# Optimization experiments

Measured on AMD Instinct MI355X. Metric: run time of the kernel, lower is better.

The kernel has to match this reference:

```python
import jax, jax.numpy as jnp
import numpy as np
import math

B, S, HID, H = 4, 2048, 1024, 16
D = HID // H


def setup_inputs() -> dict:
    key = jax.random.key(0)
    ks = jax.random.split(key, 13)
    xavier = lambda k: jax.random.normal(k, (HID, HID), jnp.float32) * math.sqrt(2.0 / (HID + HID))
    return {
        "q": jax.random.normal(ks[0], (B, S, HID), jnp.float32),
        "k": jax.random.normal(ks[1], (B, S, HID), jnp.float32),
        "v": jax.random.normal(ks[2], (B, S, HID), jnp.float32),
        "padding_mask": jax.random.randint(ks[3], (B, S), 0, 2, jnp.int32),
        "Wq": xavier(ks[4]), "bq": jnp.zeros((HID,), jnp.float32),
        "Wk": xavier(ks[5]), "bk": jnp.zeros((HID,), jnp.float32),
        "Wv": xavier(ks[6]), "bv": jnp.zeros((HID,), jnp.float32),
        "Wo": xavier(ks[7]), "bo": jnp.zeros((HID,), jnp.float32),
        "is_causal": 1,
    }


def reference(q, k, v, padding_mask, Wq, bq, Wk, bk, Wv, bv, Wo, bo, is_causal):
    b, s, _ = q.shape
    # torch Linear: y = x @ W.T + b; reshape to [B, H, S, D]
    proj = lambda x, W, bias: (x @ W.T + bias).reshape(b, s, H, D).transpose(0, 2, 1, 3)
    qh, kh, vh = proj(q, Wq, bq), proj(k, Wk, bk), proj(v, Wv, bv)
    corr = jnp.einsum("bhqd,bhkd->bhqk", qh, kh) / math.sqrt(D)  # [B,H,S,S]
    # padding_mask.view(B,1,S,1): masks QUERY rows where mask == 0 (faithful to source)
    corr = jnp.where(padding_mask[:, None, :, None] == 0, jnp.float32(-1e9), corr)
    if is_causal:
        # triu -inf above diagonal; where(...) equals corr + (-inf) at masked slots
        tri = jnp.triu(jnp.ones((s, s), bool), k=1)
        corr = jnp.where(tri[None, None], -jnp.inf, corr)
    prob = jax.nn.softmax(corr, axis=-1)  # dropout p=0 (eval)
    hidden = jnp.einsum("bhqk,bhkd->bhqd", prob, vh)  # [B,H,S,D]
    hidden = hidden.transpose(0, 2, 1, 3).reshape(b, s, H * D)
    return hidden @ Wo.T + bo
```

## Files before the change

kernel.cpp:

```cpp
#include <hip/hip_runtime.h>
#include <hip/hip_bf16.h>
#include <stdint.h>

typedef __attribute__((ext_vector_type(8))) short bf16x8;
typedef __attribute__((ext_vector_type(4))) float f32x4;
typedef __attribute__((ext_vector_type(16))) float f32x16;
typedef __attribute__((ext_vector_type(8))) unsigned short ushort8;
typedef __attribute__((ext_vector_type(4))) unsigned short ushort4v;
typedef __attribute__((ext_vector_type(4))) unsigned int u32x4;
typedef __attribute__((ext_vector_type(2))) unsigned int u32x2;

#define DEVINL __device__ __forceinline__

static constexpr int BB  = 4;
static constexpr int SS  = 2048;
static constexpr int HID = 1024;
static constexpr int NH  = 16;
static constexpr int DH  = 64;

DEVINL unsigned short f2bf(float f) {
  unsigned u = __builtin_bit_cast(unsigned, f);
  u += 0x7fffu + ((u >> 16) & 1u);
  return (unsigned short)(u >> 16);
}

DEVINL unsigned cvt_pk_bf16(float lo, float hi) {
  unsigned r;
  asm("v_cvt_pk_bf16_f32 %0, %1, %2" : "=v"(r) : "v"(lo), "v"(hi));
  return r;
}

DEVINL void gload_lds16(const void* g, void* lds) {
  __builtin_amdgcn_global_load_lds(
      (__attribute__((address_space(1))) unsigned int*)(g),
      (__attribute__((address_space(3))) unsigned int*)(lds), 16, 0, 0);
}

__global__ void cvt4_weights(const float* __restrict__ a,
                             const float* __restrict__ b,
                             const float* __restrict__ c,
                             const float* __restrict__ d,
                             unsigned short* __restrict__ dst) {
  int which = blockIdx.x >> 10;
  const float* src = which == 0 ? a : which == 1 ? b : which == 2 ? c : d;
  int i = ((blockIdx.x & 1023) * 256 + threadIdx.x) * 4;
  float4 v = *(const float4*)(src + i);
  ushort4v h;
  h.x = f2bf(v.x); h.y = f2bf(v.y); h.z = f2bf(v.z); h.w = f2bf(v.w);
  *(ushort4v*)(dst + which * 1048576 + i) = h;
}

__launch_bounds__(256)
__global__ void gemm_qkv(const float* __restrict__ qp,
                         const float* __restrict__ kp,
                         const float* __restrict__ vp,
                         const unsigned short* __restrict__ W,
                         const float* __restrict__ bq,
                         const float* __restrict__ bk,
                         const float* __restrict__ bv,
                         unsigned short* __restrict__ dstQK,
                         unsigned short* __restrict__ Vt, float sclq) {
  __shared__ __align__(16) unsigned char As[16384];
  __shared__ __align__(16) unsigned char Bs[16384];
  const int cpx = gridDim.x >> 3;
  const int bid = (blockIdx.x & 7) * cpx + (blockIdx.x >> 3);
  const int which = bid / 512;
  const int tile = bid - which * 512;
  const int bm = tile >> 3, bn = tile & 7;
  const int m0 = bm << 7, n0 = bn << 7;
  const int K = 1024, N = 1024;
  const float* Af = which == 0 ? qp : which == 1 ? kp : vp;
  const unsigned short* Bw = W + which * 1048576;
  const float* bias = which == 0 ? bq : which == 1 ? bk : bv;
  const float osc = which == 0 ? sclq : 1.0f;

  const int t = threadIdx.x, lane = t & 63, wv = t >> 6;
  const int wr = wv >> 1, wc = wv & 1;
  const int l15 = lane & 15, l4 = lane >> 4;

  f32x4 acc[4][4] = {};

  for (int k0 = 0; k0 < K; k0 += 64) {
#pragma unroll
    for (int j = 0; j < 4; ++j) {
      int p = (wv * 4 + j) * 1024 + lane * 16;
      int row = p >> 7;
      int cb = (p & 127) ^ ((row & 7) << 4);
      gload_lds16(Bw + (size_t)(n0 + row) * K + k0 + (cb >> 1),
                  Bs + (wv * 4 + j) * 1024);
    }
#pragma unroll
    for (int j = 0; j < 8; ++j) {
      int qid = t + j * 256;
      int row = qid >> 4;
      int q16 = qid & 15;
      float4 v = *(const float4*)(Af + (size_t)(m0 + row) * K + k0 + q16 * 4);
      u32x2 w;
      w.x = cvt_pk_bf16(v.x, v.y);
      w.y = cvt_pk_bf16(v.z, v.w);
      int byte = (row * 128 + q16 * 8) ^ ((row & 7) << 4);
      *(u32x2*)(As + byte) = w;
    }
    asm volatile("s_waitcnt vmcnt(0)" ::: "memory");
    __syncthreads();

    bf16x8 af[2][4], bfr[2][4];
#pragma unroll
    for (int kh = 0; kh < 2; ++kh) {
#pragma unroll
      for (int m = 0; m < 4; ++m) {
        int r = wr * 64 + m * 16 + l15;
        int byte = (r * 128 + kh * 64 + l4 * 16) ^ ((r & 7) << 4);
        af[kh][m] = *(const bf16x8*)(As + byte);
      }
#pragma unroll
      for (int n = 0; n < 4; ++n) {
        int r = wc * 64 + n * 16 + l15;
        int byte = (r * 128 + kh * 64 + l4 * 16) ^ ((r & 7) << 4);
        bfr[kh][n] = *(const bf16x8*)(Bs + byte);
      }
    }
#pragma unroll
    for (int kh = 0; kh < 2; ++kh)
#pragma unroll
      for (int m = 0; m < 4; ++m)
#pragma unroll
        for (int n = 0; n < 4; ++n)
          acc[m][n] = __builtin_amdgcn_mfma_f32_16x16x32_bf16(
              af[kh][m], bfr[kh][n], acc[m][n], 0, 0, 0);
    __syncthreads();
  }

  if (which < 2) {
    unsigned short* Cp = dstQK + (size_t)which * 8388608;
#pragma unroll
    for (int n = 0; n < 4; ++n) {
      int col = n0 + wc * 64 + n * 16 + l15;
      float bc = bias[col];
#pragma unroll
      for (int m = 0; m < 4; ++m) {
        int rowb = m0 + wr * 64 + m * 16 + l4 * 4;
#pragma unroll
        for (int r = 0; r < 4; ++r) {
          float val = (acc[m][n][r] + bc) * osc;
          Cp[(size_t)(rowb + r) * N + col] = f2bf(val);
        }
      }
    }
  } else {
#pragma unroll
    for (int n = 0; n < 4; ++n) {
      int dcol = n0 + wc * 64 + n * 16 + l15;
      float bc = bias[dcol];
#pragma unroll
      for (int m = 0; m < 4; ++m) {
        int srow = m0 + wr * 64 + m * 16 + l4 * 4;
        int bb = srow >> 11, s = srow & 2047;
        ushort4v o;
#pragma unroll
        for (int r = 0; r < 4; ++r) o[r] = f2bf(acc[m][n][r] + bc);
        *(ushort4v*)(Vt + ((size_t)(bb * 1024 + dcol)) * 2048 + s) = o;
      }
    }
  }
}

__launch_bounds__(256)
__global__ void gemm_out(const unsigned short* __restrict__ Ab,
                         const unsigned short* __restrict__ Bw,
                         const float* __restrict__ bias,
                         float* __restrict__ Cp, int M, int N, int K) {
  __shared__ __align__(16) unsigned char As[16384];
  __shared__ __align__(16) unsigned char Bs[16384];
  const int cpx = gridDim.x >> 3;
  const int bid = (blockIdx.x & 7) * cpx + (blockIdx.x >> 3);
  const int nb = N >> 7;
  const int bm = bid / nb, bn = bid % nb;
  const int m0 = bm << 7, n0 = bn << 7;
  const int t = threadIdx.x, lane = t & 63, wv = t >> 6;
  const int wr = wv >> 1, wc = wv & 1;
  const int l15 = lane & 15, l4 = lane >> 4;

  f32x4 acc[4][4] = {};

  for (int k0 = 0; k0 < K; k0 += 64) {
#pragma unroll
    for (int j = 0; j < 4; ++j) {
      int p = (wv * 4 + j) * 1024 + lane * 16;
      int row = p >> 7;
      int cb = (p & 127) ^ ((row & 7) << 4);
      gload_lds16(Bw + (size_t)(n0 + row) * K + k0 + (cb >> 1),
                  Bs + (wv * 4 + j) * 1024);
      gload_lds16(Ab + (size_t)(m0 + row) * K + k0 + (cb >> 1),
                  As + (wv * 4 + j) * 1024);
    }
    asm volatile("s_waitcnt vmcnt(0)" ::: "memory");
    __syncthreads();

    bf16x8 af[2][4], bfr[2][4];
#pragma unroll
    for (int kh = 0; kh < 2; ++kh) {
#pragma unroll
      for (int m = 0; m < 4; ++m) {
        int r = wr * 64 + m * 16 + l15;
        int byte = (r * 128 + kh * 64 + l4 * 16) ^ ((r & 7) << 4);
        af[kh][m] = *(const bf16x8*)(As + byte);
      }
#pragma unroll
      for (int n = 0; n < 4; ++n) {
        int r = wc * 64 + n * 16 + l15;
        int byte = (r * 128 + kh * 64 + l4 * 16) ^ ((r & 7) << 4);
        bfr[kh][n] = *(const bf16x8*)(Bs + byte);
      }
    }
#pragma unroll
    for (int kh = 0; kh < 2; ++kh)
#pragma unroll
      for (int m = 0; m < 4; ++m)
#pragma unroll
        for (int n = 0; n < 4; ++n)
          acc[m][n] = __builtin_amdgcn_mfma_f32_16x16x32_bf16(
              af[kh][m], bfr[kh][n], acc[m][n], 0, 0, 0);
    __syncthreads();
  }

#pragma unroll
  for (int n = 0; n < 4; ++n) {
    int col = n0 + wc * 64 + n * 16 + l15;
    float bc = bias[col];
#pragma unroll
    for (int m = 0; m < 4; ++m) {
      int rowb = m0 + wr * 64 + m * 16 + l4 * 4;
#pragma unroll
      for (int r = 0; r < 4; ++r)
        Cp[(size_t)(rowb + r) * N + col] = acc[m][n][r] + bc;
    }
  }
}

__launch_bounds__(256)
__global__ void attn_kernel(const unsigned short* __restrict__ Qh,
                            const unsigned short* __restrict__ Kh,
                            const unsigned short* __restrict__ Vt,
                            const int* __restrict__ pad,
                            const int* __restrict__ pcausal,
                            unsigned short* __restrict__ Out) {
  __shared__ __align__(16) unsigned char Ks[2][16384];
  __shared__ __align__(16) unsigned char Vs[2][16384];
  const int bid = (blockIdx.x & 7) * 64 + (blockIdx.x >> 3);
  const int pr = bid & 7, h = (bid >> 3) & 15, b = bid >> 7;
  const int t = threadIdx.x, lane = t & 63, wv = t >> 6;
  const int l31 = lane & 31, hi = lane >> 5;
  const int causal = *pcausal;

  for (int half = 0; half < 2; ++half) {
    const int qt = half ? (15 - pr) : pr;
    const int q0 = qt << 7;
    const int qrow = q0 + wv * 32 + l31;
    const bool padded = (pad[b * SS + qrow] == 0);

    const unsigned short* Qb = Qh + ((size_t)(b * SS) + qrow) * HID + h * DH;
    bf16x8 qf[4];
#pragma unroll
    for (int dd = 0; dd < 4; ++dd) {
      qf[dd] = *(const bf16x8*)(Qb + dd * 16 + hi * 8);
      if (padded) qf[dd] = (bf16x8)0;
    }

    f32x16 oacc[2] = {};
    float m = -__builtin_inff(), l = 0.f;
    const int nkt = causal ? (qt + 1) : (SS >> 7);

    auto STAGE = [&](int kt, int s) {
#pragma unroll
      for (int j = 0; j < 4; ++j) {
        int p = (wv * 4 + j) * 1024 + lane * 16;
        int kr = p >> 7;
        int kcb = (p & 127) ^ ((kr & 7) << 4);
        gload_lds16(Kh + ((size_t)(b * SS) + (kt << 7) + kr) * HID + h * DH +
                        (kcb >> 1),
                    Ks[s] + (wv * 4 + j) * 1024);
        int vr = p >> 8;
        int vcb = (p & 255) ^ ((vr & 15) << 4);
        gload_lds16(Vt + ((size_t)((b * NH + h) * DH + vr)) * SS + (kt << 7) +
                        (vcb >> 1),
                    Vs[s] + (wv * 4 + j) * 1024);
      }
    };

    if (half) __syncthreads();
    STAGE(0, 0);
    for (int kt = 0; kt < nkt; ++kt) {
      asm volatile("s_waitcnt vmcnt(0)" ::: "memory");
      __syncthreads();
      if (kt + 1 < nkt) STAGE(kt + 1, (kt + 1) & 1);
      const unsigned char* Kb = Ks[kt & 1];
      const unsigned char* Vb = Vs[kt & 1];

#pragma unroll
      for (int sub = 0; sub < 2; ++sub) {
        const int k0 = (kt << 7) + (sub << 6);
        const bool active = (!causal) || (k0 <= q0 + wv * 32 + 31);
        if (!active) continue;
        f32x16 sacc[2] = {};
#pragma unroll
        for (int kb = 0; kb < 2; ++kb) {
#pragma unroll
          for (int dd = 0; dd < 4; ++dd) {
            int krow = sub * 64 + kb * 32 + l31;
            int byte = (krow * 128 + dd * 32 + hi * 16) ^ ((krow & 7) << 4);
            bf16x8 kf = *(const bf16x8*)(Kb + byte);
            sacc[kb] = __builtin_amdgcn_mfma_f32_32x32x16_bf16(kf, qf[dd],
                                                               sacc[kb], 0, 0, 0);
          }
        }
        if (causal && (k0 + 63 > q0 + wv * 32)) {
#pragma unroll
          for (int kb = 0; kb < 2; ++kb)
#pragma unroll
            for (int r = 0; r < 16; ++r) {
              int kidx = k0 + kb * 32 + (r & 3) + 8 * (r >> 2) + 4 * hi;
              if (kidx > qrow) sacc[kb][r] = -__builtin_inff();
            }
        }
        float ta = fmaxf(sacc[0][0], sacc[0][1]);
        float tb = fmaxf(sacc[0][2], sacc[0][3]);
#pragma unroll
        for (int r = 4; r < 16; r += 4) {
          ta = fmaxf(ta, fmaxf(sacc[0][r], sacc[0][r + 1]));
          tb = fmaxf(tb, fmaxf(sacc[0][r + 2], sacc[0][r + 3]));
        }
#pragma unroll
        for (int r = 0; r < 16; r += 4) {
          ta = fmaxf(ta, fmaxf(sacc[1][r], sacc[1][r + 1]));
          tb = fmaxf(tb, fmaxf(sacc[1][r + 2], sacc[1][r + 3]));
        }
        float tmax = fmaxf(ta, tb);
        tmax = fmaxf(tmax, __shfl_xor(tmax, 32));
        if (__any(tmax > m + 8.0f)) {
          float mnew = fmaxf(m, tmax);
          float corr = __builtin_amdgcn_exp2f(m - mnew);
          m = mnew;
          l *= corr;
#pragma unroll
          for (int db = 0; db < 2; ++db)
#pragma unroll
            for (int r = 0; r < 16; ++r) oacc[db][r] *= corr;
        }
        float ls = 0.f;
#pragma unroll
        for (int kb = 0; kb < 2; ++kb)
#pragma unroll
          for (int r = 0; r < 16; ++r) {
            float p = __builtin_amdgcn_exp2f(sacc[kb][r] - m);
            sacc[kb][r] = p;
            ls += p;
          }
        l += ls;

        bf16x8 pf[4];
#pragma unroll
        for (int kb = 0; kb < 2; ++kb) {
          unsigned w0 = cvt_pk_bf16(sacc[kb][0], sacc[kb][1]);
          unsigned w1 = cvt_pk_bf16(sacc[kb][2], sacc[kb][3]);
          unsigned w2 = cvt_pk_bf16(sacc[kb][4], sacc[kb][5]);
          unsigned w3 = cvt_pk_bf16(sacc[kb][6], sacc[kb][7]);
          unsigned w4 = cvt_pk_bf16(sacc[kb][8], sacc[kb][9]);
          unsigned w5 = cvt_pk_bf16(sacc[kb][10], sacc[kb][11]);
          unsigned w6 = cvt_pk_bf16(sacc[kb][12], sacc[kb][13]);
          unsigned w7 = cvt_pk_bf16(sacc[kb][14], sacc[kb][15]);
          unsigned t0 = __shfl_xor(hi ? w0 : w2, 32);
          unsigned t1 = __shfl_xor(hi ? w1 : w3, 32);
          unsigned t2 = __shfl_xor(hi ? w4 : w6, 32);
          unsigned t3 = __shfl_xor(hi ? w5 : w7, 32);
          u32x4 lo, hf;
          lo[0] = hi ? t0 : w0;
          lo[1] = hi ? t1 : w1;
          lo[2] = hi ? w2 : t0;
          lo[3] = hi ? w3 : t1;
          hf[0] = hi ? t2 : w4;
          hf[1] = hi ? t3 : w5;
          hf[2] = hi ? w6 : t2;
          hf[3] = hi ? w7 : t3;
          pf[2 * kb] = __builtin_bit_cast(bf16x8, lo);
          pf[2 * kb + 1] = __builtin_bit_cast(bf16x8, hf);
        }
#pragma unroll
        for (int db = 0; db < 2; ++db) {
#pragma unroll
          for (int kk = 0; kk < 4; ++kk) {
            int drow = db * 32 + l31;
            int byte = (drow * 256 + sub * 128 + kk * 32 + hi * 16) ^
                       ((drow & 15) << 4);
            bf16x8 vf = *(const bf16x8*)(Vb + byte);
            oacc[db] = __builtin_amdgcn_mfma_f32_32x32x16_bf16(vf, pf[kk],
                                                               oacc[db], 0, 0, 0);
          }
        }
      }
    }

    float ltot = l + __shfl_xor(l, 32);
    float inv = 1.0f / ltot;
    size_t rowoff = ((size_t)(b * SS) + qrow) * HID + h * DH;
#pragma unroll
    for (int db = 0; db < 2; ++db) {
#pragma unroll
      for (int g = 0; g < 4; ++g) {
        ushort4v o;
#pragma unroll
        for (int j = 0; j < 4; ++j) o[j] = f2bf(oacc[db][4 * g + j] * inv);
        *(ushort4v*)(Out + rowoff + db * 32 + 8 * g + 4 * hi) = o;
      }
    }
  }
}

extern "C" void kernel_launch(void* const* d_in, const int* in_sizes, int n_in,
                              void* d_out, int out_size, void* d_ws,
                              size_t ws_size, hipStream_t stream) {
  const float* q = (const float*)d_in[0];
  const float* k = (const float*)d_in[1];
  const float* v = (const float*)d_in[2];
  const int* pad = (const int*)d_in[3];
  const float* Wq = (const float*)d_in[4];
  const float* bq = (const float*)d_in[5];
  const float* Wk = (const float*)d_in[6];
  const float* bk = (const float*)d_in[7];
  const float* Wv = (const float*)d_in[8];
  const float* bv = (const float*)d_in[9];
  const float* Wo = (const float*)d_in[10];
  const float* bo = (const float*)d_in[11];
  const int* iscausal = (const int*)d_in[12];
  float* out = (float*)d_out;

  const float SCL = 0.18033688011112042f;
  const int NQKV = BB * SS * HID;

  unsigned short* Wcat = (unsigned short*)d_ws;
  unsigned short* Wob = Wcat + 3145728;
  unsigned short* Qh = Wob + 1048576;
  unsigned short* Kh = Qh + (size_t)NQKV;
  unsigned short* Vtp = Kh + (size_t)NQKV;
  unsigned short* Htmp = Vtp + (size_t)NQKV;

  cvt4_weights<<<4096, 256, 0, stream>>>(Wq, Wk, Wv, Wo, Wcat);

  gemm_qkv<<<1536, 256, 0, stream>>>(q, k, v, Wcat, bq, bk, bv, Qh, Vtp, SCL);

  attn_kernel<<<512, 256, 0, stream>>>(Qh, Kh, Vtp, pad, iscausal, Htmp);

  gemm_out<<<512, 256, 0, stream>>>(Htmp, Wob, bo, out, 8192, 1024, 1024);
}
```

Baseline: 183.5 us.

## Software-pipeline QKV GEMM with register-prefetched A and double-buffered B tiles

The QKV projection GEMM now prefetches the next fp32 A tile into registers and issues the next B tile's direct-to-LDS loads into a second LDS buffer while the current tile is being multiplied. A partial vmcnt wait lets the current tile's loads retire while the next ones stay in flight. This hides global-load latency behind MFMA work, at the cost of 16KB more LDS and 32 more VGPRs for the staged A data, which may lower occupancy. The hand-counted vmcnt(12) must match the number of outstanding loads exactly, or the kernel will read incomplete data.

```diff
diff --git a/kernel.cpp b/kernel.cpp
--- a/kernel.cpp
+++ b/kernel.cpp
@@ -61,7 +61,7 @@
                          unsigned short* __restrict__ dstQK,
                          unsigned short* __restrict__ Vt, float sclq) {
   __shared__ __align__(16) unsigned char As[16384];
-  __shared__ __align__(16) unsigned char Bs[16384];
+  __shared__ __align__(16) unsigned char Bs[2][16384];
   const int cpx = gridDim.x >> 3;
   const int bid = (blockIdx.x & 7) * cpx + (blockIdx.x >> 3);
   const int which = bid / 512;
@@ -79,30 +79,55 @@
   const int l15 = lane & 15, l4 = lane >> 4;
 
   f32x4 acc[4][4] = {};
-
-  for (int k0 = 0; k0 < K; k0 += 64) {
+  float4 ar[8];
+
+  auto LOAD_A = [&](int k0) {
+#pragma unroll
+    for (int j = 0; j < 8; ++j) {
+      int qid = t + j * 256;
+      int row = qid >> 4;
+      int q16 = qid & 15;
+      ar[j] = *(const float4*)(Af + (size_t)(m0 + row) * K + k0 + q16 * 4);
+    }
+  };
+  auto WRITE_A = [&]() {
+#pragma unroll
+    for (int j = 0; j < 8; ++j) {
+      int qid = t + j * 256;
+      int row = qid >> 4;
+      int q16 = qid & 15;
+      u32x2 w;
+      w.x = cvt_pk_bf16(ar[j].x, ar[j].y);
+      w.y = cvt_pk_bf16(ar[j].z, ar[j].w);
+      int byte = (row * 128 + q16 * 8) ^ ((row & 7) << 4);
+      *(u32x2*)(As + byte) = w;
+    }
+  };
+  auto STAGE_B = [&](int k0, int s) {
 #pragma unroll
     for (int j = 0; j < 4; ++j) {
       int p = (wv * 4 + j) * 1024 + lane * 16;
       int row = p >> 7;
       int cb = (p & 127) ^ ((row & 7) << 4);
       gload_lds16(Bw + (size_t)(n0 + row) * K + k0 + (cb >> 1),
-                  Bs + (wv * 4 + j) * 1024);
-    }
-#pragma unroll
-    for (int j = 0; j < 8; ++j) {
-      int qid = t + j * 256;
-      int row = qid >> 4;
-      int q16 = qid & 15;
-      float4 v = *(const float4*)(Af + (size_t)(m0 + row) * K + k0 + q16 * 4);
-      u32x2 w;
-      w.x = cvt_pk_bf16(v.x, v.y);
-      w.y = cvt_pk_bf16(v.z, v.w);
-      int byte = (row * 128 + q16 * 8) ^ ((row & 7) << 4);
-      *(u32x2*)(As + byte) = w;
-    }
-    asm volatile("s_waitcnt vmcnt(0)" ::: "memory");
-    __syncthreads();
+                  Bs[s] + (wv * 4 + j) * 1024);
+    }
+  };
+
+  LOAD_A(0);
+  STAGE_B(0, 0);
+  const int nk = K >> 6;
+  for (int i = 0; i < nk; ++i) {
+    const int s = i & 1;
+    WRITE_A();
+    if (i + 1 < nk) {
+      LOAD_A((i + 1) << 6);
+      STAGE_B((i + 1) << 6, s ^ 1);
+      asm volatile("s_waitcnt vmcnt(12) lgkmcnt(0)" ::: "memory");
+    } else {
+      asm volatile("s_waitcnt vmcnt(0) lgkmcnt(0)" ::: "memory");
+    }
+    __builtin_amdgcn_s_barrier();
 
     bf16x8 af[2][4], bfr[2][4];
 #pragma unroll
@@ -117,7 +142,7 @@
       for (int n = 0; n < 4; ++n) {
         int r = wc * 64 + n * 16 + l15;
         int byte = (r * 128 + kh * 64 + l4 * 16) ^ ((r & 7) << 4);
-        bfr[kh][n] = *(const bf16x8*)(Bs + byte);
+        bfr[kh][n] = *(const bf16x8*)(Bs[s] + byte);
       }
     }
 #pragma unroll
@@ -128,7 +153,9 @@
         for (int n = 0; n < 4; ++n)
           acc[m][n] = __builtin_amdgcn_mfma_f32_16x16x32_bf16(
               af[kh][m], bfr[kh][n], acc[m][n], 0, 0, 0);
-    __syncthreads();
+
+    asm volatile("s_waitcnt lgkmcnt(0)" ::: "memory");
+    __builtin_amdgcn_s_barrier();
   }
 
   if (which < 2) {
```

Measured after the change: 181.4 us. No clear change (-1.1%).
